# Optimization experiments

Hardware: AMD Instinct MI355X
Metric: run time of the kernel (lower is better)

Reference implementation:

```python
import jax, jax.numpy as jnp
import numpy as np

L1, L2, B, D1, D2, HEADS, M = 1024, 1024, 8, 512, 1024, 16, 1024
DPH = M // HEADS  # 64


def setup_inputs() -> dict:
    key = jax.random.key(0)
    ks = jax.random.split(key, 10)
    w = lambda k, shp: jax.random.normal(k, shp, jnp.float32) * 0.02
    z = lambda n: jnp.zeros((n,), jnp.float32)
    return {
        "ctx_1": jax.random.normal(ks[0], (L1, B, D1), jnp.float32),
        "ctx_2": jax.random.normal(ks[1], (L2, B, D2), jnp.float32),
        "Wk1": w(ks[2], (M, D1)), "bk1": z(M),
        "Wv1": w(ks[3], (M, D1)), "bv1": z(M),
        "Wk2": w(ks[4], (M, D2)), "bk2": z(M),
        "Wv2": w(ks[5], (M, D2)), "bv2": z(M),
        "Wf12": w(ks[6], (M, M)), "bf12": z(M),
        "Wf21": w(ks[7], (M, M)), "bf21": z(M),
    }


def _shape_heads(x):
    # [L, B, M] -> [B, H, L, dph]
    L, Bs, _ = x.shape
    return x.reshape(L, Bs, HEADS, DPH).transpose(1, 2, 0, 3)


def _unshape(x):
    # [B, H, L, dph] -> [L, B, M]
    Bs, Hn, L, d = x.shape
    return x.transpose(2, 0, 1, 3).reshape(L, Bs, Hn * d)


def reference(ctx_1, ctx_2, Wk1, bk1, Wv1, bv1, Wk2, bk2, Wv2, bv2,
              Wf12, bf12, Wf21, bf21):
    k1 = _shape_heads(ctx_1 @ Wk1.T + bk1)  # [B,H,L1,d]
    v1 = _shape_heads(ctx_1 @ Wv1.T + bv1)  # [B,H,L1,d]
    k2 = _shape_heads(ctx_2 @ Wk2.T + bk2)  # [B,H,L2,d]
    v2 = _shape_heads(ctx_2 @ Wv2.T + bv2)  # [B,H,L2,d]

    # scores: key_2 @ key_1^T -> [B, H, L2, L1]
    scores = jnp.einsum('bhqd,bhkd->bhqk', k2, k1)

    # direction 1 -> 2: softmax over dim=2 (the L2 axis), then AV with value_1
    dist_1_to_2 = jax.nn.softmax(scores, axis=2)
    context_1_to_2 = jnp.einsum('bhqk,bhkd->bhqd', dist_1_to_2, v1)  # [B,H,L2,d]
    context_1_to_2 = _unshape(context_1_to_2) @ Wf12.T + bf12        # [L2,B,M]

    # direction 2 -> 1: softmax over dim=1 (the head axis), transpose, AV with value_2
    dist_2_to_1 = jax.nn.softmax(scores, axis=1)
    context_2_to_1 = jnp.einsum('bhqk,bhqd->bhkd', dist_2_to_1, v2)  # [B,H,L1,d]
    context_2_to_1 = _unshape(context_2_to_1) @ Wf21.T + bf21        # [L1,B,M]

    return (context_2_to_1, context_1_to_2)
```

## Files before the change

kernel.cpp:

```cpp
#include <hip/hip_runtime.h>
#include <hip/hip_bf16.h>

constexpr int LQ  = 1024;
constexpr int BN  = 8;
constexpr int D1N = 512;
constexpr int D2N = 1024;
constexpr int HN  = 16;
constexpr int MN  = 1024;
constexpr int DPH = 64;

typedef __attribute__((ext_vector_type(8)))  short bf16x8;
typedef __attribute__((ext_vector_type(2)))  float f32x2;
typedef __attribute__((ext_vector_type(4)))  float f32x4;
typedef __attribute__((ext_vector_type(16))) float f32x16;

__device__ __forceinline__ unsigned short f2bf(float f) {
  unsigned u = __float_as_uint(f);
  u += 0x7FFFu + ((u >> 16) & 1u);
  return (unsigned short)(u >> 16);
}
__device__ __forceinline__ float bf2f(unsigned short u) {
  return __uint_as_float(((unsigned)u) << 16);
}
__device__ __forceinline__ float rcpf(float x) {
  float r;
  asm("v_rcp_f32 %0, %1" : "=v"(r) : "v"(x));
  return r;
}

__device__ __forceinline__ f32x4 mfma16(bf16x8 a, bf16x8 b, f32x4 c) {
  return __builtin_amdgcn_mfma_f32_16x16x32_bf16(a, b, c, 0, 0, 0);
}
__device__ __forceinline__ f32x16 mfma32(bf16x8 a, bf16x8 b, f32x16 c) {
  return __builtin_amdgcn_mfma_f32_32x32x16_bf16(a, b, c, 0, 0, 0);
}
__device__ __forceinline__ f32x16 zero16() {
  f32x16 z;
#pragma unroll
  for (int i = 0; i < 16; ++i) z[i] = 0.f;
  return z;
}

__device__ __forceinline__ unsigned cvtpk(float lo, float hi) {
  unsigned r;
  asm("v_cvt_pk_bf16_f32 %0, %1, %2" : "=v"(r) : "v"(lo), "v"(hi));
  return r;
}

__device__ __forceinline__ void lds_barrier() {
  asm volatile("s_waitcnt lgkmcnt(0)" ::: "memory");
  __builtin_amdgcn_s_barrier();
}

__device__ __forceinline__ bf16x8 pfrag(const float* p) {
  unsigned x0 = cvtpk(p[0], p[1]), y0 = cvtpk(p[4], p[5]);
  unsigned x1 = cvtpk(p[2], p[3]), y1 = cvtpk(p[6], p[7]);
  asm volatile("v_permlane32_swap_b32 %0, %1" : "+v"(x0), "+v"(y0));
  asm volatile("v_permlane32_swap_b32 %0, %1" : "+v"(x1), "+v"(y1));
  union { unsigned u[4]; bf16x8 v; } r;
  r.u[0] = x0; r.u[1] = x1; r.u[2] = y0; r.u[3] = y1;
  return r.v;
}

__device__ __forceinline__ bf16x8 pack8(f32x4 p0, f32x4 p1) {
  bf16x8 o;
  o[0] = (short)f2bf(p0[0]); o[1] = (short)f2bf(p0[1]);
  o[2] = (short)f2bf(p0[2]); o[3] = (short)f2bf(p0[3]);
  o[4] = (short)f2bf(p1[0]); o[5] = (short)f2bf(p1[1]);
  o[6] = (short)f2bf(p1[2]); o[7] = (short)f2bf(p1[3]);
  return o;
}
__device__ __forceinline__ bf16x8 pack8q(f32x4 lo, f32x4 hi) {
  union { unsigned u[4]; bf16x8 v; } r;
  r.u[0] = cvtpk(lo[0], lo[1]); r.u[1] = cvtpk(lo[2], lo[3]);
  r.u[2] = cvtpk(hi[0], hi[1]); r.u[3] = cvtpk(hi[2], hi[3]);
  return r.v;
}

__global__ __launch_bounds__(256) void cvt_kernel(const float* __restrict__ src,
                                                  unsigned short* __restrict__ dst,
                                                  int n8) {
  int i = blockIdx.x * blockDim.x + threadIdx.x;
  if (i >= n8) return;
  const f32x4* s = (const f32x4*)src;
  f32x4 x = s[2 * i], y = s[2 * i + 1];
  ((bf16x8*)dst)[i] = pack8(x, y);
}

template <int K, int MODE, bool AF32>
__device__ __forceinline__ void gemm_body(const void* __restrict__ Ap,
                                          const unsigned short* __restrict__ W,
                                          const float* __restrict__ bias,
                                          void* __restrict__ outp,
                                          int rowb, int colb) {
  __shared__ unsigned short As[128 * 40], Bs[128 * 40];
  const int tid = threadIdx.x, wave = tid >> 6, lane = tid & 63;
  const int lg = lane >> 4, lm = lane & 15;
  const int wrow = (wave >> 1) * 64, wcol = (wave & 1) * 64;
  const int sr = tid >> 1, sh = (tid & 1) * 16;
  const unsigned short* Arow = AF32 ? nullptr
      : (const unsigned short*)Ap + (size_t)(rowb + sr) * K + sh;
  const float* ArowF = AF32 ? (const float*)Ap + (size_t)(rowb + sr) * K + sh
                            : nullptr;
  const unsigned short* Wrow = W + (size_t)(colb + sr) * K + sh;

  f32x4 acc[4][4];
#pragma unroll
  for (int i = 0; i < 4; ++i)
#pragma unroll
    for (int j = 0; j < 4; ++j) acc[i][j] = (f32x4){0.f, 0.f, 0.f, 0.f};

  f32x4 fa0, fa1, fa2, fa3;
  bf16x8 a0, a1, b0, b1;
  if (AF32) {
    fa0 = *(const f32x4*)(ArowF);     fa1 = *(const f32x4*)(ArowF + 4);
    fa2 = *(const f32x4*)(ArowF + 8); fa3 = *(const f32x4*)(ArowF + 12);
  } else {
    a0 = *(const bf16x8*)(Arow);
    a1 = *(const bf16x8*)(Arow + 8);
  }
  b0 = *(const bf16x8*)(Wrow);
  b1 = *(const bf16x8*)(Wrow + 8);

  for (int kk = 0; kk < K; kk += 32) {
    lds_barrier();
    if (AF32) {
      *(bf16x8*)&As[sr * 40 + sh]     = pack8q(fa0, fa1);
      *(bf16x8*)&As[sr * 40 + sh + 8] = pack8q(fa2, fa3);
    } else {
      *(bf16x8*)&As[sr * 40 + sh] = a0;
      *(bf16x8*)&As[sr * 40 + sh + 8] = a1;
    }
    *(bf16x8*)&Bs[sr * 40 + sh] = b0;
    *(bf16x8*)&Bs[sr * 40 + sh + 8] = b1;
    const int kn = (kk + 32 < K) ? kk + 32 : 0;
    if (AF32) {
      fa0 = *(const f32x4*)(ArowF + kn);     fa1 = *(const f32x4*)(ArowF + kn + 4);
      fa2 = *(const f32x4*)(ArowF + kn + 8); fa3 = *(const f32x4*)(ArowF + kn + 12);
    } else {
      a0 = *(const bf16x8*)(Arow + kn);
      a1 = *(const bf16x8*)(Arow + kn + 8);
    }
    b0 = *(const bf16x8*)(Wrow + kn);
    b1 = *(const bf16x8*)(Wrow + kn + 8);
    lds_barrier();
    bf16x8 af[4], wf[4];
#pragma unroll
    for (int i = 0; i < 4; ++i) af[i] = *(const bf16x8*)&As[(wrow + i * 16 + lm) * 40 + lg * 8];
#pragma unroll
    for (int j = 0; j < 4; ++j) wf[j] = *(const bf16x8*)&Bs[(wcol + j * 16 + lm) * 40 + lg * 8];
#pragma unroll
    for (int i = 0; i < 4; ++i)
#pragma unroll
      for (int j = 0; j < 4; ++j) acc[i][j] = mfma16(af[i], wf[j], acc[i][j]);
  }

#pragma unroll
  for (int j = 0; j < 4; ++j) {
    int col = colb + wcol + j * 16 + lm;
    float bs = bias[col];
#pragma unroll
    for (int i = 0; i < 4; ++i) {
#pragma unroll
      for (int r = 0; r < 4; ++r) {
        int row = rowb + wrow + i * 16 + lg * 4 + r;
        float v = acc[i][j][r] + bs;
        if (MODE == 0) {
          int l = row >> 3, bb = row & 7, h = col >> 6, d = col & 63;
          ((unsigned short*)outp)[(((size_t)(bb * HN + h)) * LQ + l) * DPH + d] = f2bf(v);
        } else {
          ((float*)outp)[(size_t)row * MN + col] = v;
        }
      }
    }
  }
}

template <int K>
__global__ __launch_bounds__(256) void gemm_pair_f32_kernel(
    const float* __restrict__ A,
    const unsigned short* __restrict__ W0, const unsigned short* __restrict__ W1,
    const float* __restrict__ b0, const float* __restrict__ b1,
    void* __restrict__ o0, void* __restrict__ o1) {
  const int sel = blockIdx.y >> 3;
  gemm_body<K, 0, true>(A, sel ? W1 : W0, sel ? b1 : b0, sel ? o1 : o0,
                        blockIdx.x * 128, (blockIdx.y & 7) * 128);
}

template <int K>
__global__ __launch_bounds__(256) void gemm_dual_kernel(
    const unsigned short* __restrict__ A0, const unsigned short* __restrict__ A1,
    const unsigned short* __restrict__ W0, const unsigned short* __restrict__ W1,
    const float* __restrict__ b0, const float* __restrict__ b1,
    void* __restrict__ o0, void* __restrict__ o1) {
  const int sel = blockIdx.y >> 3;
  gemm_body<K, 2, false>(sel ? A1 : A0, sel ? W1 : W0, sel ? b1 : b0,
                         sel ? o1 : o0, blockIdx.x * 128, (blockIdx.y & 7) * 128);
}

__global__ __launch_bounds__(256) void transpose_kernel(const unsigned short* __restrict__ V,
                                                        unsigned short* __restrict__ VT,
                                                        const float* __restrict__ scale) {
  __shared__ unsigned short t[64][72];
  int bh = blockIdx.y, l0 = blockIdx.x * 64;
  int tid = threadIdx.x;
  int r = tid >> 2, c0 = (tid & 3) * 16;
  const unsigned short* src = V + ((size_t)bh * LQ + l0 + r) * DPH + c0;
  bf16x8 v0 = *(const bf16x8*)(src);
  bf16x8 v1 = *(const bf16x8*)(src + 8);
  if (scale) {
    float sc = scale[(size_t)bh * LQ + l0 + r];
#pragma unroll
    for (int j = 0; j < 8; ++j) {
      v0[j] = (short)f2bf(bf2f((unsigned short)v0[j]) * sc);
      v1[j] = (short)f2bf(bf2f((unsigned short)v1[j]) * sc);
    }
  }
  *(bf16x8*)&t[r][c0] = v0;
  *(bf16x8*)&t[r][c0 + 8] = v1;
  __syncthreads();
  int d = tid >> 2, lc = (tid & 3) * 16;
  bf16x8 o0, o1;
#pragma unroll
  for (int j = 0; j < 8; ++j) {
    o0[j] = (short)t[lc + j][d];
    o1[j] = (short)t[lc + 8 + j][d];
  }
  unsigned short* dst = VT + ((size_t)bh * DPH + d) * LQ + l0 + lc;
  *(bf16x8*)dst = o0;
  *(bf16x8*)(dst + 8) = o1;
}

__global__ __launch_bounds__(256) void col_reduce_kernel(const unsigned short* __restrict__ K1p,
                                                         const unsigned short* __restrict__ K2p,
                                                         float* __restrict__ inv_colsum) {
  int bh = blockIdx.x, kb = blockIdx.y * 128;
  int wave = threadIdx.x >> 6, lane = threadIdx.x & 63, l31 = lane & 31, sg = lane >> 5;
  int k0w = kb + wave * 32;
  const unsigned short* k1 = K1p + (size_t)bh * LQ * DPH;
  const unsigned short* k2 = K2p + (size_t)bh * LQ * DPH;
  bf16x8 bk[4];
#pragma unroll
  for (int i = 0; i < 4; ++i)
    bk[i] = *(const bf16x8*)(k1 + (size_t)(k0w + l31) * DPH + i * 16 + sg * 8);
  float tot = 0.f;
  for (int q0 = 0; q0 < LQ; q0 += 32) {
    bf16x8 aq[4];
#pragma unroll
    for (int i = 0; i < 4; ++i)
      aq[i] = *(const bf16x8*)(k2 + (size_t)(q0 + l31) * DPH + i * 16 + sg * 8);
    f32x16 cs = zero16();
#pragma unroll
    for (int i = 0; i < 4; ++i) cs = mfma32(aq[i], bk[i], cs);
#pragma unroll
    for (int r = 0; r < 16; ++r) tot += __expf(cs[r]);
  }
  tot += __shfl_xor(tot, 32);
  if (lane < 32) inv_colsum[(size_t)bh * LQ + k0w + lane] = 1.0f / tot;
}

__global__ __launch_bounds__(256) void ctx12_kernel(const unsigned short* __restrict__ K1p,
                                                    const unsigned short* __restrict__ K2p,
                                                    const unsigned short* __restrict__ V1Ts,
                                                    unsigned short* __restrict__ c12) {
  int bh = blockIdx.x, b = bh >> 4, h = bh & 15;
  int wave = threadIdx.x >> 6, lane = threadIdx.x & 63, l31 = lane & 31, sg = lane >> 5;
  int q0 = blockIdx.y * 128 + wave * 32;
  const unsigned short* k1 = K1p + (size_t)bh * LQ * DPH;
  const unsigned short* k2 = K2p + (size_t)bh * LQ * DPH;
  const unsigned short* vt = V1Ts + (size_t)bh * DPH * LQ;

  bf16x8 bq[4];
#pragma unroll
  for (int i = 0; i < 4; ++i)
    bq[i] = *(const bf16x8*)(k2 + (size_t)(q0 + l31) * DPH + i * 16 + sg * 8);

  f32x16 acc0 = zero16(), acc1 = zero16();
  for (int k0 = 0; k0 < LQ; k0 += 32) {
    bf16x8 ak[4];
#pragma unroll
    for (int i = 0; i < 4; ++i)
      ak[i] = *(const bf16x8*)(k1 + (size_t)(k0 + l31) * DPH + i * 16 + sg * 8);
    f32x16 cs = zero16();
#pragma unroll
    for (int i = 0; i < 4; ++i) cs = mfma32(ak[i], bq[i], cs);
    float p[16];
#pragma unroll
    for (int r = 0; r < 16; ++r) p[r] = __expf(cs[r]);
    bf16x8 pa0 = pfrag(p), pa1 = pfrag(p + 8);
    bf16x8 v00 = *(const bf16x8*)(vt + (size_t)l31 * LQ + k0 + sg * 8);
    bf16x8 v01 = *(const bf16x8*)(vt + (size_t)l31 * LQ + k0 + 16 + sg * 8);
    bf16x8 v10 = *(const bf16x8*)(vt + (size_t)(32 + l31) * LQ + k0 + sg * 8);
    bf16x8 v11 = *(const bf16x8*)(vt + (size_t)(32 + l31) * LQ + k0 + 16 + sg * 8);
    acc0 = mfma32(pa0, v00, acc0);
    acc0 = mfma32(pa1, v01, acc0);
    acc1 = mfma32(pa0, v10, acc1);
    acc1 = mfma32(pa1, v11, acc1);
  }
#pragma unroll
  for (int r = 0; r < 16; ++r) {
    int q = q0 + (r & 3) + 8 * (r >> 2) + 4 * sg;
    size_t base = ((size_t)q * BN + b) * MN + h * 64;
    c12[base + l31] = f2bf(acc0[r]);
    c12[base + 32 + l31] = f2bf(acc1[r]);
  }
}

__global__ __launch_bounds__(1024) void ctx21_fused_kernel(const unsigned short* __restrict__ K1p,
                                                           const unsigned short* __restrict__ K2p,
                                                           const unsigned short* __restrict__ V2T,
                                                           unsigned short* __restrict__ c21) {
  constexpr int SP = 34;
  constexpr int WS = 32 * SP;
  __shared__ float strip[16 * WS];
  __shared__ float tot[WS];
  const int b = blockIdx.x, kb = blockIdx.y;
  const int tid = threadIdx.x, wave = tid >> 6, lane = tid & 63;
  const int l31 = lane & 31, sg = lane >> 5;
  const int h = wave, bh = b * HN + h;
  const int k0 = kb * 32;
  const unsigned short* k1 = K1p + (size_t)bh * LQ * DPH;
  const unsigned short* k2 = K2p + (size_t)bh * LQ * DPH;
  const unsigned short* vt = V2T + (size_t)bh * DPH * LQ;
  float* mystrip = &strip[wave * WS];

  const int bk_ = tid & 31, bq2 = (tid >> 5) * 2;

  bf16x8 bk[4];
#pragma unroll
  for (int i = 0; i < 4; ++i)
    bk[i] = *(const bf16x8*)(k1 + (size_t)(k0 + l31) * DPH + i * 16 + sg * 8);

  bf16x8 aq[4];
#pragma unroll
  for (int i = 0; i < 4; ++i)
    aq[i] = *(const bf16x8*)(k2 + (size_t)(l31) * DPH + i * 16 + sg * 8);

  f32x16 acc0 = zero16(), acc1 = zero16();

  for (int t = 0; t < LQ / 32; ++t) {
    const int q0 = t * 32;
    f32x16 cs = zero16();
#pragma unroll
    for (int i = 0; i < 4; ++i) cs = mfma32(aq[i], bk[i], cs);
    const int qn = ((t + 1) & 31) * 32;
#pragma unroll
    for (int i = 0; i < 4; ++i)
      aq[i] = *(const bf16x8*)(k2 + (size_t)(qn + l31) * DPH + i * 16 + sg * 8);
    float pex[16];
#pragma unroll
    for (int r = 0; r < 16; ++r) pex[r] = __expf(cs[r]);
#pragma unroll
    for (int g = 0; g < 4; ++g) {
      int qb = g * 8 + 4 * sg;
      *(f32x2*)&mystrip[l31 * SP + qb]     = (f32x2){pex[4 * g],     pex[4 * g + 1]};
      *(f32x2*)&mystrip[l31 * SP + qb + 2] = (f32x2){pex[4 * g + 2], pex[4 * g + 3]};
    }
    bf16x8 v00 = *(const bf16x8*)(vt + (size_t)l31 * LQ + q0 + sg * 8);
    bf16x8 v01 = *(const bf16x8*)(vt + (size_t)l31 * LQ + q0 + 16 + sg * 8);
    bf16x8 v10 = *(const bf16x8*)(vt + (size_t)(32 + l31) * LQ + q0 + sg * 8);
    bf16x8 v11 = *(const bf16x8*)(vt + (size_t)(32 + l31) * LQ + q0 + 16 + sg * 8);
    lds_barrier();
    if (tid < 512) {
      int off = bk_ * SP + bq2;
      f32x2 s = *(const f32x2*)&strip[off];
#pragma unroll
      for (int w = 1; w < 16; ++w) {
        f32x2 v = *(const f32x2*)&strip[w * WS + off];
        s.x += v.x; s.y += v.y;
      }
      f32x2 rc; rc.x = rcpf(s.x); rc.y = rcpf(s.y);
      *(f32x2*)&tot[off] = rc;
    }
    lds_barrier();
    float p8a[8], p8b[8];
#pragma unroll
    for (int g = 0; g < 4; ++g) {
      int qb = g * 8 + 4 * sg;
      f32x2 t0 = *(const f32x2*)&tot[l31 * SP + qb];
      f32x2 t1 = *(const f32x2*)&tot[l31 * SP + qb + 2];
      float* dstp = (g < 2) ? &p8a[(g & 1) * 4] : &p8b[(g & 1) * 4];
      dstp[0] = pex[4 * g]     * t0.x;
      dstp[1] = pex[4 * g + 1] * t0.y;
      dstp[2] = pex[4 * g + 2] * t1.x;
      dstp[3] = pex[4 * g + 3] * t1.y;
    }
    bf16x8 pa0 = pfrag(p8a), pa1 = pfrag(p8b);
    acc0 = mfma32(pa0, v00, acc0);
    acc0 = mfma32(pa1, v01, acc0);
    acc1 = mfma32(pa0, v10, acc1);
    acc1 = mfma32(pa1, v11, acc1);
  }
#pragma unroll
  for (int r = 0; r < 16; ++r) {
    int k = k0 + (r & 3) + 8 * (r >> 2) + 4 * sg;
    size_t base = ((size_t)k * BN + b) * MN + h * 64;
    c21[base + l31] = f2bf(acc0[r]);
    c21[base + 32 + l31] = f2bf(acc1[r]);
  }
}

extern "C" void kernel_launch(void* const* d_in, const int* in_sizes, int n_in,
                              void* d_out, int out_size, void* d_ws, size_t ws_size,
                              hipStream_t stream) {
  const float* ctx1 = (const float*)d_in[0];
  const float* ctx2 = (const float*)d_in[1];
  const float* Wk1 = (const float*)d_in[2];  const float* bk1 = (const float*)d_in[3];
  const float* Wv1 = (const float*)d_in[4];  const float* bv1 = (const float*)d_in[5];
  const float* Wk2 = (const float*)d_in[6];  const float* bk2 = (const float*)d_in[7];
  const float* Wv2 = (const float*)d_in[8];  const float* bv2 = (const float*)d_in[9];
  const float* Wf12 = (const float*)d_in[10]; const float* bf12 = (const float*)d_in[11];
  const float* Wf21 = (const float*)d_in[12]; const float* bf21 = (const float*)d_in[13];

  char* ws = (char*)d_ws;
  size_t off = 0;
  auto alloc = [&](size_t bytes) {
    void* p = ws + off;
    off += (bytes + 255) & ~(size_t)255;
    return p;
  };
  const size_t KV_BYTES = (size_t)BN * HN * LQ * DPH * 2;

  unsigned short* wk1b = (unsigned short*)alloc((size_t)MN * D1N * 2);
  unsigned short* wv1b = (unsigned short*)alloc((size_t)MN * D1N * 2);
  unsigned short* wk2b = (unsigned short*)alloc((size_t)MN * D2N * 2);
  unsigned short* wv2b = (unsigned short*)alloc((size_t)MN * D2N * 2);
  unsigned short* wf12b = (unsigned short*)alloc((size_t)MN * MN * 2);
  unsigned short* wf21b = (unsigned short*)alloc((size_t)MN * MN * 2);
  unsigned short* K1buf = (unsigned short*)alloc(KV_BYTES);
  unsigned short* K2buf = (unsigned short*)alloc(KV_BYTES);
  unsigned short* V1T = (unsigned short*)alloc(KV_BYTES);
  unsigned short* V2T = (unsigned short*)alloc(KV_BYTES);
  float* invcs = (float*)alloc((size_t)BN * HN * LQ * 4);
  unsigned short* c12 = (unsigned short*)alloc(KV_BYTES);
  unsigned short* c21 = (unsigned short*)alloc(KV_BYTES);
  unsigned short* V1tmp = c12;
  unsigned short* V2tmp = c21;

  auto cvt = [&](const float* s, unsigned short* d, int n) {
    int n8 = n / 8;
    cvt_kernel<<<(n8 + 255) / 256, 256, 0, stream>>>(s, d, n8);
  };
  cvt(Wk1, wk1b, MN * D1N);
  cvt(Wv1, wv1b, MN * D1N);
  cvt(Wk2, wk2b, MN * D2N);
  cvt(Wv2, wv2b, MN * D2N);
  cvt(Wf12, wf12b, MN * MN);
  cvt(Wf21, wf21b, MN * MN);

  gemm_pair_f32_kernel<D1N><<<dim3(64, 16), 256, 0, stream>>>(
      ctx1, wk1b, wv1b, bk1, bv1, K1buf, V1tmp);
  gemm_pair_f32_kernel<D2N><<<dim3(64, 16), 256, 0, stream>>>(
      ctx2, wk2b, wv2b, bk2, bv2, K2buf, V2tmp);

  col_reduce_kernel<<<dim3(BN * HN, LQ / 128), 256, 0, stream>>>(K1buf, K2buf, invcs);
  dim3 gt(LQ / 64, BN * HN);
  transpose_kernel<<<gt, 256, 0, stream>>>(V1tmp, V1T, invcs);
  transpose_kernel<<<gt, 256, 0, stream>>>(V2tmp, V2T, nullptr);

  ctx12_kernel<<<dim3(BN * HN, LQ / 128), 256, 0, stream>>>(K1buf, K2buf, V1T, c12);
  ctx21_fused_kernel<<<dim3(BN, LQ / 32), 1024, 0, stream>>>(K1buf, K2buf, V2T, c21);

  float* out0 = (float*)d_out;
  float* out1 = out0 + (size_t)LQ * BN * MN;
  gemm_dual_kernel<MN><<<dim3(64, 16), 256, 0, stream>>>(
      c21, c12, wf21b, wf12b, bf21, bf12, out0, out1);
}
```

Before: 476.0 us.

## Split ctx21 fused kernel over query halves with bf16 LDS strips and add pass

Splits the ctx21 kernel's 1024-step query loop into two halves launched as a grid z dimension, so twice as many blocks exist to fill the GPU. Each half writes a bf16 partial result to a new workspace, and a new add-and-convert kernel sums the two partials into c21. The per-wave exp strip in shared memory is now stored as bf16 instead of fp32, which shrinks LDS use so more blocks can stay resident, and the cross-head reduction uses 256 threads handling four columns each. The cost is an extra kernel launch, extra global traffic for the partials, and lower precision from rounding the partials and softmax denominators to bf16.

```diff
diff --git a/kernel.cpp b/kernel.cpp
--- a/kernel.cpp
+++ b/kernel.cpp
@@ -10,6 +10,7 @@
 constexpr int DPH = 64;
 
 typedef __attribute__((ext_vector_type(8)))  short bf16x8;
+typedef __attribute__((ext_vector_type(4)))  short bf16x4;
 typedef __attribute__((ext_vector_type(2)))  float f32x2;
 typedef __attribute__((ext_vector_type(4)))  float f32x4;
 typedef __attribute__((ext_vector_type(16))) float f32x16;
@@ -85,6 +86,21 @@
   const f32x4* s = (const f32x4*)src;
   f32x4 x = s[2 * i], y = s[2 * i + 1];
   ((bf16x8*)dst)[i] = pack8(x, y);
+}
+
+__global__ __launch_bounds__(256) void addcvt_kernel(const unsigned short* __restrict__ p0,
+                                                     const unsigned short* __restrict__ p1,
+                                                     unsigned short* __restrict__ dst,
+                                                     int n8) {
+  int i = blockIdx.x * blockDim.x + threadIdx.x;
+  if (i >= n8) return;
+  bf16x8 a = ((const bf16x8*)p0)[i];
+  bf16x8 b = ((const bf16x8*)p1)[i];
+  bf16x8 o;
+#pragma unroll
+  for (int j = 0; j < 8; ++j)
+    o[j] = (short)f2bf(bf2f((unsigned short)a[j]) + bf2f((unsigned short)b[j]));
+  ((bf16x8*)dst)[i] = o;
 }
 
 template <int K, int MODE, bool AF32>
@@ -306,15 +322,16 @@
   }
 }
 
-__global__ __launch_bounds__(1024) void ctx21_fused_kernel(const unsigned short* __restrict__ K1p,
-                                                           const unsigned short* __restrict__ K2p,
-                                                           const unsigned short* __restrict__ V2T,
-                                                           unsigned short* __restrict__ c21) {
-  constexpr int SP = 34;
-  constexpr int WS = 32 * SP;
-  __shared__ float strip[16 * WS];
-  __shared__ float tot[WS];
-  const int b = blockIdx.x, kb = blockIdx.y;
+__global__ __launch_bounds__(1024, 8) void ctx21_part_kernel(const unsigned short* __restrict__ K1p,
+                                                             const unsigned short* __restrict__ K2p,
+                                                             const unsigned short* __restrict__ V2T,
+                                                             unsigned short* __restrict__ part) {
+  constexpr int SPB = 36;
+  constexpr int WSB = 32 * SPB;
+  constexpr int SPT = 36;
+  __shared__ unsigned short stripb[16 * WSB];
+  __shared__ float tot[32 * SPT];
+  const int b = blockIdx.x, kb = blockIdx.y, qh = blockIdx.z;
   const int tid = threadIdx.x, wave = tid >> 6, lane = tid & 63;
   const int l31 = lane & 31, sg = lane >> 5;
   const int h = wave, bh = b * HN + h;
@@ -322,9 +339,10 @@
   const unsigned short* k1 = K1p + (size_t)bh * LQ * DPH;
   const unsigned short* k2 = K2p + (size_t)bh * LQ * DPH;
   const unsigned short* vt = V2T + (size_t)bh * DPH * LQ;
-  float* mystrip = &strip[wave * WS];
-
-  const int bk_ = tid & 31, bq2 = (tid >> 5) * 2;
+  unsigned short* mystrip = &stripb[wave * WSB];
+
+  const int tbeg = qh * 16, tend = tbeg + 16;
+  const int bk_ = tid & 31, bq4 = (tid >> 5) * 4;
 
   bf16x8 bk[4];
 #pragma unroll
@@ -334,11 +352,11 @@
   bf16x8 aq[4];
 #pragma unroll
   for (int i = 0; i < 4; ++i)
-    aq[i] = *(const bf16x8*)(k2 + (size_t)(l31) * DPH + i * 16 + sg * 8);
+    aq[i] = *(const bf16x8*)(k2 + (size_t)(tbeg * 32 + l31) * DPH + i * 16 + sg * 8);
 
   f32x16 acc0 = zero16(), acc1 = zero16();
 
-  for (int t = 0; t < LQ / 32; ++t) {
+  for (int t = tbeg; t < tend; ++t) {
     const int q0 = t * 32;
     f32x16 cs = zero16();
 #pragma unroll
@@ -353,32 +371,37 @@
 #pragma unroll
     for (int g = 0; g < 4; ++g) {
       int qb = g * 8 + 4 * sg;
-      *(f32x2*)&mystrip[l31 * SP + qb]     = (f32x2){pex[4 * g],     pex[4 * g + 1]};
-      *(f32x2*)&mystrip[l31 * SP + qb + 2] = (f32x2){pex[4 * g + 2], pex[4 * g + 3]};
+      *(unsigned*)&mystrip[l31 * SPB + qb]     = cvtpk(pex[4 * g],     pex[4 * g + 1]);
+      *(unsigned*)&mystrip[l31 * SPB + qb + 2] = cvtpk(pex[4 * g + 2], pex[4 * g + 3]);
     }
     bf16x8 v00 = *(const bf16x8*)(vt + (size_t)l31 * LQ + q0 + sg * 8);
     bf16x8 v01 = *(const bf16x8*)(vt + (size_t)l31 * LQ + q0 + 16 + sg * 8);
     bf16x8 v10 = *(const bf16x8*)(vt + (size_t)(32 + l31) * LQ + q0 + sg * 8);
     bf16x8 v11 = *(const bf16x8*)(vt + (size_t)(32 + l31) * LQ + q0 + 16 + sg * 8);
     lds_barrier();
-    if (tid < 512) {
-      int off = bk_ * SP + bq2;
-      f32x2 s = *(const f32x2*)&strip[off];
-#pragma unroll
-      for (int w = 1; w < 16; ++w) {
-        f32x2 v = *(const f32x2*)&strip[w * WS + off];
-        s.x += v.x; s.y += v.y;
+    if (tid < 256) {
+      int off = bk_ * SPB + bq4;
+      f32x4 s = (f32x4){0.f, 0.f, 0.f, 0.f};
+#pragma unroll
+      for (int w = 0; w < 16; ++w) {
+        bf16x4 v = *(const bf16x4*)&stripb[w * WSB + off];
+        s[0] += bf2f((unsigned short)v[0]);
+        s[1] += bf2f((unsigned short)v[1]);
+        s[2] += bf2f((unsigned short)v[2]);
+        s[3] += bf2f((unsigned short)v[3]);
       }
-      f32x2 rc; rc.x = rcpf(s.x); rc.y = rcpf(s.y);
-      *(f32x2*)&tot[off] = rc;
+      f32x4 rc;
+#pragma unroll
+      for (int j = 0; j < 4; ++j) rc[j] = rcpf(s[j]);
+      *(f32x4*)&tot[bk_ * SPT + bq4] = rc;
     }
     lds_barrier();
     float p8a[8], p8b[8];
 #pragma unroll
     for (int g = 0; g < 4; ++g) {
       int qb = g * 8 + 4 * sg;
-      f32x2 t0 = *(const f32x2*)&tot[l31 * SP + qb];
-      f32x2 t1 = *(const f32x2*)&tot[l31 * SP + qb + 2];
+      f32x2 t0 = *(const f32x2*)&tot[l31 * SPT + qb];
+      f32x2 t1 = *(const f32x2*)&tot[l31 * SPT + qb + 2];
       float* dstp = (g < 2) ? &p8a[(g & 1) * 4] : &p8b[(g & 1) * 4];
       dstp[0] = pex[4 * g]     * t0.x;
       dstp[1] = pex[4 * g + 1] * t0.y;
@@ -391,12 +414,13 @@
     acc1 = mfma32(pa0, v10, acc1);
     acc1 = mfma32(pa1, v11, acc1);
   }
+  unsigned short* dst = part + (size_t)qh * (8192 * (size_t)MN);
 #pragma unroll
   for (int r = 0; r < 16; ++r) {
     int k = k0 + (r & 3) + 8 * (r >> 2) + 4 * sg;
     size_t base = ((size_t)k * BN + b) * MN + h * 64;
-    c21[base + l31] = f2bf(acc0[r]);
-    c21[base + 32 + l31] = f2bf(acc1[r]);
+    dst[base + l31] = f2bf(acc0[r]);
+    dst[base + 32 + l31] = f2bf(acc1[r]);
   }
 }
 
@@ -434,6 +458,7 @@
   float* invcs = (float*)alloc((size_t)BN * HN * LQ * 4);
   unsigned short* c12 = (unsigned short*)alloc(KV_BYTES);
   unsigned short* c21 = (unsigned short*)alloc(KV_BYTES);
+  unsigned short* c21p = (unsigned short*)alloc((size_t)2 * 8192 * MN * 2);
   unsigned short* V1tmp = c12;
   unsigned short* V2tmp = c21;
 
@@ -459,7 +484,9 @@
   transpose_kernel<<<gt, 256, 0, stream>>>(V2tmp, V2T, nullptr);
 
   ctx12_kernel<<<dim3(BN * HN, LQ / 128), 256, 0, stream>>>(K1buf, K2buf, V1T, c12);
-  ctx21_fused_kernel<<<dim3(BN, LQ / 32), 1024, 0, stream>>>(K1buf, K2buf, V2T, c21);
+  ctx21_part_kernel<<<dim3(BN, LQ / 32, 2), 1024, 0, stream>>>(K1buf, K2buf, V2T, c21p);
+  addcvt_kernel<<<(8192 * MN / 8 + 255) / 256, 256, 0, stream>>>(
+      c21p, c21p + (size_t)8192 * MN, c21, 8192 * MN / 8);
 
   float* out0 = (float*)d_out;
   float* out1 = out0 + (size_t)LQ * BN * MN;
```

Measured after the change: 879.7 us. 1.85x slower.
